# Optimization experiments

Hardware: AMD Instinct MI355X
Metric: run time of the kernel (lower is better)

The kernel has to match this reference:

```python
import jax, jax.numpy as jnp
import numpy as np

B, C, H, W = 32, 3, 224, 224
P = 16                 # patch size
D = 768                # embed_size
NH = 12                # num heads
HD = D // NH           # head size
L = 12                 # depth
MLP = 4 * D
NC = 1000              # num classes
GH, GW = H // P, W // P
T = GH * GW            # tokens = 196
PATCH_DIM = P * P * C
EPS = 1e-5


def posemb_sincos_2d(h, w, dim, temperature=10000.0):
    yy, xx = jnp.meshgrid(jnp.arange(h, dtype=jnp.float32),
                          jnp.arange(w, dtype=jnp.float32), indexing='ij')
    omega = jnp.arange(dim // 4, dtype=jnp.float32) / (dim // 4 - 1)
    omega = 1.0 / (temperature ** omega)
    yv = yy.reshape(-1)[:, None] * omega[None, :]
    xv = xx.reshape(-1)[:, None] * omega[None, :]
    return jnp.concatenate([jnp.sin(xv), jnp.cos(xv), jnp.sin(yv), jnp.cos(yv)], axis=1)


def layernorm(x, g, b):
    mu = jnp.mean(x, axis=-1, keepdims=True)
    var = jnp.mean((x - mu) ** 2, axis=-1, keepdims=True)
    return (x - mu) * jax.lax.rsqrt(var + EPS) * g + b


def setup_inputs() -> dict:
    key = jax.random.key(0)
    ks = jax.random.split(key, 16)
    s = 0.02
    inp = {
        'x': jax.random.normal(ks[0], (B, C, H, W), jnp.float32),
        'embed_W': jax.random.normal(ks[1], (PATCH_DIM, D), jnp.float32) * s,
        'embed_b': jnp.zeros((D,), jnp.float32),
        'Wq': jax.random.normal(ks[2], (L, NH, D, HD), jnp.float32) * s,
        'Wk': jax.random.normal(ks[3], (L, NH, D, HD), jnp.float32) * s,
        'Wv': jax.random.normal(ks[4], (L, NH, D, HD), jnp.float32) * s,
        'Wo': jax.random.normal(ks[5], (L, D, D), jnp.float32) * s,
        'bo': jnp.zeros((L, D), jnp.float32),
        'ln1_g': jnp.ones((L, D), jnp.float32),
        'ln1_b': jnp.zeros((L, D), jnp.float32),
        'ln2_g': jnp.ones((L, D), jnp.float32),
        'ln2_b': jnp.zeros((L, D), jnp.float32),
        'W1': jax.random.normal(ks[6], (L, D, MLP), jnp.float32) * s,
        'b1': jnp.zeros((L, MLP), jnp.float32),
        'W2': jax.random.normal(ks[7], (L, MLP, D), jnp.float32) * s,
        'b2': jnp.zeros((L, D), jnp.float32),
        'head_W': jax.random.normal(ks[8], (D, NC), jnp.float32) * s,
    }
    return inp


def reference(x, embed_W, embed_b, Wq, Wk, Wv, Wo, bo,
              ln1_g, ln1_b, ln2_g, ln2_b, W1, b1, W2, b2, head_W):
    # patchify: b c (h p1) (w p2) -> b (h w) (p1 p2 c)
    p = x.reshape(B, C, GH, P, GW, P)
    p = p.transpose(0, 2, 4, 3, 5, 1).reshape(B, T, PATCH_DIM)
    h = p @ embed_W + embed_b + posemb_sincos_2d(GH, GW, D)[None]  # [B,T,D]

    scale = HD ** -0.5
    for l in range(L):
        xn = layernorm(h, ln1_g[l], ln1_b[l])
        q = jnp.einsum('btd,hde->bhte', xn, Wq[l])
        k = jnp.einsum('btd,hde->bhte', xn, Wk[l])
        v = jnp.einsum('btd,hde->bhte', xn, Wv[l])
        scores = jax.nn.softmax(jnp.einsum('bhte,bhse->bhts', q, k) * scale, axis=-1)
        att = jnp.einsum('bhts,bhse->bhte', scores, v)
        att = att.transpose(0, 2, 1, 3).reshape(B, T, D)  # concat heads
        h = h + att @ Wo[l] + bo[l]
        xn = layernorm(h, ln2_g[l], ln2_b[l])
        h = h + jax.nn.gelu(xn @ W1[l] + b1[l], approximate=False) @ W2[l] + b2[l]

    return h.mean(axis=1) @ head_W  # [B, NC]
```

## Files before the change

kernel.cpp:

```cpp
#include <hip/hip_runtime.h>
#include <cstdint>


typedef __bf16 bf16_t;
typedef __bf16 bf16x8 __attribute__((ext_vector_type(8)));
typedef __bf16 bf16x4 __attribute__((ext_vector_type(4)));
typedef float  f32x4  __attribute__((ext_vector_type(4)));

#define NLAYER 12
#define BMPAD 56
#define PSTRIDE 4816896l

__device__ __forceinline__ void g2lds16(const void* g, void* l) {
  __builtin_amdgcn_global_load_lds(
      (const __attribute__((address_space(1))) void*)g,
      (__attribute__((address_space(3))) void*)l, 16, 0, 0);
}

__global__ __launch_bounds__(256) void tcvt(
    const float* __restrict__ in, bf16_t* __restrict__ out,
    int R, int C, long inStride, long outOuter, long outInner, int innerN)
{
  int bi = blockIdx.z;
  in  += (long)bi * inStride;
  out += (long)(bi / innerN) * outOuter + (long)(bi % innerN) * outInner;
  __shared__ float t[32][33];
  int c0 = blockIdx.x * 32, r0 = blockIdx.y * 32;
  int tx = threadIdx.x, ty = threadIdx.y;
  #pragma unroll
  for (int i = ty; i < 32; i += 8) {
    int r = r0 + i, c = c0 + tx;
    if (r < R && c < C) t[i][tx] = in[(long)r * C + c];
  }
  __syncthreads();
  #pragma unroll
  for (int i = ty; i < 32; i += 8) {
    int c = c0 + i, r = r0 + tx;
    if (r < R && c < C) out[(long)c * R + r] = (bf16_t)t[tx][i];
  }
}

__global__ __launch_bounds__(256) void patchify(
    const float* __restrict__ x, bf16_t* __restrict__ patches)
{
  int idx = blockIdx.x * 256 + threadIdx.x;
  int bt = idx / 768, pd = idx % 768;
  int b = bt / 196, t = bt % 196;
  int gh = t / 14, gw = t % 14;
  int p1 = pd / 48, rem = pd % 48;
  int p2 = rem / 3, c = rem % 3;
  float v = x[(((long)(b * 3 + c) * 224) + gh * 16 + p1) * 224 + gw * 16 + p2];
  patches[idx] = (bf16_t)v;
}

__global__ __launch_bounds__(256) void hinit(
    const float* __restrict__ eb, float* __restrict__ h)
{
  int idx = blockIdx.x * 256 + threadIdx.x;
  int t = idx / 768, d = idx % 768;
  int gh = t / 14, gw = t % 14;
  int quadrant = d / 192, i = d % 192;
  float omega = powf(10000.0f, -(float)i / 191.0f);
  float arg = (quadrant < 2 ? (float)gw : (float)gh) * omega;
  float pv = ((quadrant & 1) == 0) ? sinf(arg) : cosf(arg);
  float v = pv + eb[d];
  #pragma unroll
  for (int b = 0; b < 32; ++b) h[(long)b * 150528 + idx] = v;
}

__global__ __launch_bounds__(256) void ln_fuse(
    float* __restrict__ h, const bf16_t* __restrict__ pbuf, int nparts,
    const float* __restrict__ bias, const float* __restrict__ g,
    const float* __restrict__ bb, bf16_t* __restrict__ xn)
{
  int row = blockIdx.x * 4 + (threadIdx.x >> 6);
  int lane = threadIdx.x & 63;
  float* hr = h + (long)row * 768;
  const bf16_t* pr = pbuf + (long)row * 768;
  float4 v[3];
  float s = 0.f, s2 = 0.f;
  #pragma unroll
  for (int i = 0; i < 3; ++i) {
    int c4 = lane + 64 * i;
    float4 hv = ((const float4*)hr)[c4];
    float4 acc = {0.f, 0.f, 0.f, 0.f};
    for (int pp = 0; pp < nparts; ++pp) {
      bf16x4 q = *(const bf16x4*)(pr + (long)pp * PSTRIDE + c4 * 4);
      acc.x += (float)q[0]; acc.y += (float)q[1];
      acc.z += (float)q[2]; acc.w += (float)q[3];
    }
    if (bias) {
      float4 bv = ((const float4*)bias)[c4];
      acc.x += bv.x; acc.y += bv.y; acc.z += bv.z; acc.w += bv.w;
    }
    hv.x += acc.x; hv.y += acc.y; hv.z += acc.z; hv.w += acc.w;
    ((float4*)hr)[c4] = hv;
    v[i] = hv;
    s  += hv.x + hv.y + hv.z + hv.w;
    s2 += hv.x * hv.x + hv.y * hv.y + hv.z * hv.z + hv.w * hv.w;
  }
  #pragma unroll
  for (int d = 1; d < 64; d <<= 1) {
    s  += __shfl_xor(s, d, 64);
    s2 += __shfl_xor(s2, d, 64);
  }
  float mu = s * (1.0f / 768.0f);
  float var = s2 * (1.0f / 768.0f) - mu * mu;
  float rs = rsqrtf(var + 1e-5f);
  uint2* outv = (uint2*)(xn + (long)row * 768);
  const float4* gv = (const float4*)g;
  const float4* bv2 = (const float4*)bb;
  #pragma unroll
  for (int i = 0; i < 3; ++i) {
    int c4 = lane + 64 * i;
    float4 gg = gv[c4], b4 = bv2[c4];
    union { bf16_t q[4]; uint2 u; } pk;
    pk.q[0] = (bf16_t)((v[i].x - mu) * rs * gg.x + b4.x);
    pk.q[1] = (bf16_t)((v[i].y - mu) * rs * gg.y + b4.y);
    pk.q[2] = (bf16_t)((v[i].z - mu) * rs * gg.z + b4.z);
    pk.q[3] = (bf16_t)((v[i].w - mu) * rs * gg.w + b4.w);
    outv[c4] = pk.u;
  }
}

__device__ __forceinline__ float gelu_fast(float x) {
  float y = 0.7978845608f * (x + 0.044715f * x * x * x);
  float e = __expf(2.0f * y);
  float t = 1.0f - 2.0f / (e + 1.0f);
  return 0.5f * x * (1.0f + t);
}

template <int EPI, int KTOT, int KS>
__global__ __launch_bounds__(256, 4) void gemm_bt(
    const bf16_t* __restrict__ A, const bf16_t* __restrict__ Bt,
    int ldc, int Mstore, int Nstore,
    const float* __restrict__ bias,
    float* __restrict__ fout, bf16_t* __restrict__ bout)
{
  int lin = blockIdx.x;
  int bm = lin % BMPAD;
  if (bm * 128 >= Mstore) return;
  int rest = lin / BMPAD;
  int ks = rest % KS;
  int bn = rest / KS;
  constexpr int Ksl = KTOT / KS;
  int k0 = ks * Ksl;

  __shared__ __align__(16) bf16_t As[128 * 32];
  __shared__ __align__(16) bf16_t Bs[128 * 32];
  int tid = threadIdx.x;
  int wave = tid >> 6, lane = tid & 63, quad = lane >> 4, l16 = lane & 15;
  int wm = wave >> 1, wn = wave & 1;
  const bf16_t* Ab = A + (long)bm * 128 * KTOT;
  const bf16_t* Bb = Bt + (long)bn * 128 * KTOT;

  f32x4 zero = {0.f, 0.f, 0.f, 0.f};
  f32x4 acc[4][4];
  #pragma unroll
  for (int i = 0; i < 4; ++i)
    #pragma unroll
    for (int j = 0; j < 4; ++j) acc[i][j] = zero;

  int f0 = tid * 16;
  int row0 = f0 >> 6;
  int ke0 = (f0 & 63) >> 1;

  for (int kt = k0; kt < k0 + Ksl; kt += 32) {
    __syncthreads();
    g2lds16(Ab + (long)row0 * KTOT + kt + ke0,        (char*)As + f0);
    g2lds16(Ab + (long)(row0 + 64) * KTOT + kt + ke0, (char*)As + f0 + 4096);
    g2lds16(Bb + (long)row0 * KTOT + kt + ke0,        (char*)Bs + f0);
    g2lds16(Bb + (long)(row0 + 64) * KTOT + kt + ke0, (char*)Bs + f0 + 4096);
    __syncthreads();

    bf16x8 af[4], bfr[4];
    #pragma unroll
    for (int i = 0; i < 4; ++i)
      af[i] = *(const bf16x8*)(As + (wm * 64 + i * 16 + l16) * 32 + quad * 8);
    #pragma unroll
    for (int j = 0; j < 4; ++j)
      bfr[j] = *(const bf16x8*)(Bs + (wn * 64 + j * 16 + l16) * 32 + quad * 8);
    #pragma unroll
    for (int i = 0; i < 4; ++i)
      #pragma unroll
      for (int j = 0; j < 4; ++j)
        acc[i][j] = __builtin_amdgcn_mfma_f32_16x16x32_bf16(af[i], bfr[j], acc[i][j], 0, 0, 0);
  }

  int m0 = bm * 128 + wm * 64, n0 = bn * 128 + wn * 64;
  #pragma unroll
  for (int i = 0; i < 4; ++i)
    #pragma unroll
    for (int j = 0; j < 4; ++j)
      #pragma unroll
      for (int r = 0; r < 4; ++r) {
        int row = m0 + i * 16 + quad * 4 + r;
        int col = n0 + j * 16 + l16;
        if (row >= Mstore || col >= Nstore) continue;
        float v = acc[i][j][r];
        if (EPI == 0) {
          bout[(long)row * ldc + col] = (bf16_t)v;
        } else if (EPI == 3) {
          bout[(long)row * ldc + col] = (bf16_t)gelu_fast(v + bias[col]);
        } else if (EPI == 4) {
          fout[(long)row * ldc + col] = v;
        } else {
          bout[(long)ks * PSTRIDE + (long)row * ldc + col] = (bf16_t)v;
        }
      }
}

__global__ __launch_bounds__(256) void vtrans(
    const bf16_t* __restrict__ qkv, bf16_t* __restrict__ Vt)
{
  int bh = blockIdx.z, b = bh / 12, h = bh % 12;
  __shared__ bf16_t t[32][33];
  int e0 = blockIdx.x * 32, s0 = blockIdx.y * 32;
  int tx = threadIdx.x, ty = threadIdx.y;
  #pragma unroll
  for (int i = ty; i < 32; i += 8) {
    int s = s0 + i;
    bf16_t v = (bf16_t)0.0f;
    if (s < 196) v = qkv[(long)(b * 196 + s) * 2304 + 1536 + h * 64 + e0 + tx];
    t[i][tx] = v;
  }
  __syncthreads();
  #pragma unroll
  for (int i = ty; i < 32; i += 8) {
    int e = e0 + i, s = s0 + tx;
    if (s < 224) Vt[(long)bh * 64 * 224 + (long)e * 224 + s] = t[tx][i];
  }
}

__global__ __launch_bounds__(64) void attn_fused(
    const bf16_t* __restrict__ qkv, const bf16_t* __restrict__ Vt,
    bf16_t* __restrict__ att)
{
  __shared__ __align__(16) bf16_t Pl[16 * 232];
  int mt = blockIdx.x, bh = blockIdx.y;
  int b = bh / 12, h = bh % 12;
  int lane = threadIdx.x, quad = lane >> 4, l16 = lane & 15;

  #pragma unroll
  for (int i = 0; i < 4; ++i) {
    int idx = lane + 64 * i;
    Pl[(idx >> 4) * 232 + 208 + (idx & 15)] = (bf16_t)0.0f;
  }

  f32x4 zero = {0.f, 0.f, 0.f, 0.f};
  f32x4 acc[13];
  #pragma unroll
  for (int nt = 0; nt < 13; ++nt) acc[nt] = zero;

  long qoff = (long)(b * 196 + mt * 16 + l16) * 2304 + h * 64;
  #pragma unroll
  for (int kk = 0; kk < 2; ++kk) {
    bf16x8 a = *(const bf16x8*)(qkv + qoff + kk * 32 + quad * 8);
    #pragma unroll
    for (int nt = 0; nt < 13; ++nt) {
      long koff = (long)(b * 196 + nt * 16 + l16) * 2304 + 768 + h * 64 + kk * 32 + quad * 8;
      bf16x8 bb = *(const bf16x8*)(qkv + koff);
      acc[nt] = __builtin_amdgcn_mfma_f32_16x16x32_bf16(a, bb, acc[nt], 0, 0, 0);
    }
  }

  float p[13][4];
  #pragma unroll
  for (int nt = 0; nt < 13; ++nt)
    #pragma unroll
    for (int r = 0; r < 4; ++r) {
      float v = acc[nt][r] * 0.125f;
      if (nt == 12 && l16 >= 4) v = -1e30f;
      p[nt][r] = v;
    }

  #pragma unroll
  for (int r = 0; r < 4; ++r) {
    float mx = -1e30f;
    #pragma unroll
    for (int nt = 0; nt < 13; ++nt) mx = fmaxf(mx, p[nt][r]);
    #pragma unroll
    for (int d = 1; d < 16; d <<= 1) mx = fmaxf(mx, __shfl_xor(mx, d, 64));
    float sm = 0.f;
    #pragma unroll
    for (int nt = 0; nt < 13; ++nt) {
      float e = __expf(p[nt][r] - mx);
      p[nt][r] = e;
      sm += e;
    }
    #pragma unroll
    for (int d = 1; d < 16; d <<= 1) sm += __shfl_xor(sm, d, 64);
    float inv = 1.0f / sm;
    #pragma unroll
    for (int nt = 0; nt < 13; ++nt) p[nt][r] *= inv;
  }

  #pragma unroll
  for (int nt = 0; nt < 13; ++nt)
    #pragma unroll
    for (int r = 0; r < 4; ++r)
      Pl[(quad * 4 + r) * 232 + nt * 16 + l16] = (bf16_t)p[nt][r];
  __syncthreads();

  f32x4 pv[4];
  #pragma unroll
  for (int nt = 0; nt < 4; ++nt) pv[nt] = zero;
  const bf16_t* Vb = Vt + (long)bh * 64 * 224;
  #pragma unroll
  for (int ks = 0; ks < 7; ++ks) {
    bf16x8 a = *(const bf16x8*)(Pl + l16 * 232 + ks * 32 + quad * 8);
    #pragma unroll
    for (int nt = 0; nt < 4; ++nt) {
      bf16x8 bb = *(const bf16x8*)(Vb + (long)(nt * 16 + l16) * 224 + ks * 32 + quad * 8);
      pv[nt] = __builtin_amdgcn_mfma_f32_16x16x32_bf16(a, bb, pv[nt], 0, 0, 0);
    }
  }

  #pragma unroll
  for (int nt = 0; nt < 4; ++nt)
    #pragma unroll
    for (int r = 0; r < 4; ++r) {
      int t = mt * 16 + quad * 4 + r;
      if (t < 196)
        att[(long)(b * 196 + t) * 768 + h * 64 + nt * 16 + l16] = (bf16_t)pv[nt][r];
    }
}

__global__ __launch_bounds__(256) void meanpool_fuse(
    const float* __restrict__ h, const bf16_t* __restrict__ pbuf,
    const float* __restrict__ bias, bf16_t* __restrict__ hm)
{
  int d = blockIdx.y * 256 + threadIdx.x;
  int b = blockIdx.x;
  float s = 0.f;
  for (int t = 0; t < 196; ++t) {
    long idx = (long)(b * 196 + t) * 768 + d;
    float v = h[idx];
    #pragma unroll
    for (int pp = 0; pp < 4; ++pp) v += (float)pbuf[idx + pp * PSTRIDE];
    s += v;
  }
  hm[b * 768 + d] = (bf16_t)(s * (1.0f / 196.0f) + bias[d]);
}

extern "C" void kernel_launch(void* const* d_in, const int* in_sizes, int n_in,
                              void* d_out, int out_size, void* d_ws, size_t ws_size,
                              hipStream_t stream)
{
  const float* x       = (const float*)d_in[0];
  const float* embed_W = (const float*)d_in[1];
  const float* embed_b = (const float*)d_in[2];
  const float* Wq      = (const float*)d_in[3];
  const float* Wk      = (const float*)d_in[4];
  const float* Wv      = (const float*)d_in[5];
  const float* Wo      = (const float*)d_in[6];
  const float* bo      = (const float*)d_in[7];
  const float* ln1_g   = (const float*)d_in[8];
  const float* ln1_b   = (const float*)d_in[9];
  const float* ln2_g   = (const float*)d_in[10];
  const float* ln2_b   = (const float*)d_in[11];
  const float* W1      = (const float*)d_in[12];
  const float* b1      = (const float*)d_in[13];
  const float* W2      = (const float*)d_in[14];
  const float* b2      = (const float*)d_in[15];
  const float* head_W  = (const float*)d_in[16];

  char* p = (char*)d_ws;
  auto carve = [&](size_t bytes) {
    char* r = p;
    p += (bytes + 255) & ~(size_t)255;
    return r;
  };
  bf16_t* embed_Wt = (bf16_t*)carve(589824ull * 2);
  bf16_t* qkvT     = (bf16_t*)carve(21233664ull * 2);
  bf16_t* WoT      = (bf16_t*)carve(7077888ull * 2);
  bf16_t* W1T      = (bf16_t*)carve(28311552ull * 2);
  bf16_t* W2T      = (bf16_t*)carve(28311552ull * 2);
  bf16_t* headWt   = (bf16_t*)carve(786432ull * 2);
  bf16_t* patches  = (bf16_t*)carve(4816896ull * 2);
  float*  h        = (float*)carve(4816896ull * 4);
  bf16_t* xn       = (bf16_t*)carve(4816896ull * 2);
  bf16_t* qkv      = (bf16_t*)carve(14487552ull * 2);
  bf16_t* Vt       = (bf16_t*)carve(5505024ull * 2);
  bf16_t* hmlp     = (bf16_t*)carve(19267584ull * 2);
  bf16_t* att      = (bf16_t*)carve(4816896ull * 2);
  bf16_t* pbuf     = (bf16_t*)carve(4ull * PSTRIDE * 2);
  bf16_t* hm       = (bf16_t*)carve(98304ull * 2);
  (void)ws_size; (void)n_in; (void)in_sizes; (void)out_size;

  dim3 tb32(32, 8);

  tcvt<<<dim3(24, 24, 1),   tb32, 0, stream>>>(embed_W, embed_Wt, 768, 768, 0, 0, 0, 1);
  tcvt<<<dim3(24, 24, 12),  tb32, 0, stream>>>(Wo, WoT, 768, 768, 589824, 589824, 0, 1);
  tcvt<<<dim3(2, 24, 144),  tb32, 0, stream>>>(Wq, qkvT,           768, 64, 49152, 1769472, 49152, 12);
  tcvt<<<dim3(2, 24, 144),  tb32, 0, stream>>>(Wk, qkvT + 589824,  768, 64, 49152, 1769472, 49152, 12);
  tcvt<<<dim3(2, 24, 144),  tb32, 0, stream>>>(Wv, qkvT + 1179648, 768, 64, 49152, 1769472, 49152, 12);
  tcvt<<<dim3(96, 24, 12),  tb32, 0, stream>>>(W1, W1T, 768, 3072, 2359296, 2359296, 0, 1);
  tcvt<<<dim3(24, 96, 12),  tb32, 0, stream>>>(W2, W2T, 3072, 768, 2359296, 2359296, 0, 1);
  tcvt<<<dim3(32, 24, 1),   tb32, 0, stream>>>(head_W, headWt, 768, 1000, 0, 0, 0, 1);

  patchify<<<18816, 256, 0, stream>>>(x, patches);
  hinit<<<588, 256, 0, stream>>>(embed_b, h);

  gemm_bt<5, 768, 2><<<BMPAD * 6 * 2, 256, 0, stream>>>(
      patches, embed_Wt, 768, 6272, 768, nullptr, nullptr, pbuf);

  for (int l = 0; l < NLAYER; ++l) {
    ln_fuse<<<1568, 256, 0, stream>>>(
        h, pbuf, l == 0 ? 2 : 4, l == 0 ? nullptr : b2 + (l - 1) * 768,
        ln1_g + l * 768, ln1_b + l * 768, xn);
    gemm_bt<0, 768, 1><<<BMPAD * 18, 256, 0, stream>>>(
        xn, qkvT + (long)l * 1769472, 2304, 6272, 2304,
        nullptr, nullptr, qkv);
    vtrans<<<dim3(2, 7, 384), tb32, 0, stream>>>(qkv, Vt);
    attn_fused<<<dim3(13, 384), 64, 0, stream>>>(qkv, Vt, att);
    gemm_bt<5, 768, 2><<<BMPAD * 6 * 2, 256, 0, stream>>>(
        att, WoT + (long)l * 589824, 768, 6272, 768,
        nullptr, nullptr, pbuf);
    ln_fuse<<<1568, 256, 0, stream>>>(
        h, pbuf, 2, bo + l * 768, ln2_g + l * 768, ln2_b + l * 768, xn);
    gemm_bt<3, 768, 1><<<BMPAD * 24, 256, 0, stream>>>(
        xn, W1T + (long)l * 2359296, 3072, 6272, 3072,
        b1 + l * 3072, nullptr, hmlp);
    gemm_bt<5, 3072, 4><<<BMPAD * 6 * 4, 256, 0, stream>>>(
        hmlp, W2T + (long)l * 2359296, 768, 6272, 768,
        nullptr, nullptr, pbuf);
  }

  meanpool_fuse<<<dim3(32, 3), 256, 0, stream>>>(h, pbuf, b2 + 11 * 768, hm);
  gemm_bt<4, 768, 1><<<BMPAD * 8, 256, 0, stream>>>(
      hm, headWt, 1000, 32, 1000, nullptr, (float*)d_out, nullptr);
}
```

Measured before the change: 3.556 ms.

## Double GEMM K-tile to 64 and XOR-swizzle LDS layout

```diff
diff --git a/kernel.cpp b/kernel.cpp
--- a/kernel.cpp
+++ b/kernel.cpp
@@ -146,8 +146,8 @@
   constexpr int Ksl = KTOT / KS;
   int k0 = ks * Ksl;
 
-  __shared__ __align__(16) bf16_t As[128 * 32];
-  __shared__ __align__(16) bf16_t Bs[128 * 32];
+  __shared__ __align__(16) bf16_t As[128 * 64];
+  __shared__ __align__(16) bf16_t Bs[128 * 64];
   int tid = threadIdx.x;
   int wave = tid >> 6, lane = tid & 63, quad = lane >> 4, l16 = lane & 15;
   int wm = wave >> 1, wn = wave & 1;
@@ -161,30 +161,47 @@
     #pragma unroll
     for (int j = 0; j < 4; ++j) acc[i][j] = zero;
 
-  int f0 = tid * 16;
-  int row0 = f0 >> 6;
-  int ke0 = (f0 & 63) >> 1;
-
-  for (int kt = k0; kt < k0 + Ksl; kt += 32) {
+  int srow = tid >> 3;
+  int sgcol = ((tid & 7) ^ (srow & 7)) * 8;
+  int ldst = tid * 16;
+
+  int aoff[2][4], boff[2][4];
+  #pragma unroll
+  for (int kh = 0; kh < 2; ++kh)
+    #pragma unroll
+    for (int i = 0; i < 4; ++i) {
+      int ra = wm * 64 + i * 16 + l16;
+      int rb = wn * 64 + i * 16 + l16;
+      int pa = ((kh * 4 + quad) ^ (ra & 7)) * 8;
+      int pb = ((kh * 4 + quad) ^ (rb & 7)) * 8;
+      aoff[kh][i] = ra * 64 + pa;
+      boff[kh][i] = rb * 64 + pb;
+    }
+
+  for (int kt = k0; kt < k0 + Ksl; kt += 64) {
     __syncthreads();
-    g2lds16(Ab + (long)row0 * KTOT + kt + ke0,        (char*)As + f0);
-    g2lds16(Ab + (long)(row0 + 64) * KTOT + kt + ke0, (char*)As + f0 + 4096);
-    g2lds16(Bb + (long)row0 * KTOT + kt + ke0,        (char*)Bs + f0);
-    g2lds16(Bb + (long)(row0 + 64) * KTOT + kt + ke0, (char*)Bs + f0 + 4096);
+    #pragma unroll
+    for (int c = 0; c < 4; ++c) {
+      g2lds16(Ab + (long)(c * 32 + srow) * KTOT + kt + sgcol,
+              (char*)As + c * 4096 + ldst);
+      g2lds16(Bb + (long)(c * 32 + srow) * KTOT + kt + sgcol,
+              (char*)Bs + c * 4096 + ldst);
+    }
     __syncthreads();
 
-    bf16x8 af[4], bfr[4];
-    #pragma unroll
-    for (int i = 0; i < 4; ++i)
-      af[i] = *(const bf16x8*)(As + (wm * 64 + i * 16 + l16) * 32 + quad * 8);
-    #pragma unroll
-    for (int j = 0; j < 4; ++j)
-      bfr[j] = *(const bf16x8*)(Bs + (wn * 64 + j * 16 + l16) * 32 + quad * 8);
-    #pragma unroll
-    for (int i = 0; i < 4; ++i)
+    #pragma unroll
+    for (int kh = 0; kh < 2; ++kh) {
+      bf16x8 af[4], bfr[4];
       #pragma unroll
-      for (int j = 0; j < 4; ++j)
-        acc[i][j] = __builtin_amdgcn_mfma_f32_16x16x32_bf16(af[i], bfr[j], acc[i][j], 0, 0, 0);
+      for (int i = 0; i < 4; ++i) af[i] = *(const bf16x8*)(As + aoff[kh][i]);
+      #pragma unroll
+      for (int j = 0; j < 4; ++j) bfr[j] = *(const bf16x8*)(Bs + boff[kh][j]);
+      #pragma unroll
+      for (int i = 0; i < 4; ++i)
+        #pragma unroll
+        for (int j = 0; j < 4; ++j)
+          acc[i][j] = __builtin_amdgcn_mfma_f32_16x16x32_bf16(af[i], bfr[j], acc[i][j], 0, 0, 0);
+    }
   }
 
   int m0 = bm * 128 + wm * 64, n0 = bn * 128 + wn * 64;
```

After: 3.292 ms. 7.4% less time.

## Double-buffer GEMM LDS with XOR swizzle and fuse V transpose into QKV epilogue

Applied to the files above, without the earlier changes.

```diff
diff --git a/kernel.cpp b/kernel.cpp
--- a/kernel.cpp
+++ b/kernel.cpp
@@ -66,6 +66,13 @@
   float v = pv + eb[d];
   #pragma unroll
   for (int b = 0; b < 32; ++b) h[(long)b * 150528 + idx] = v;
+}
+
+__global__ __launch_bounds__(256) void vpad(bf16_t* __restrict__ Vt)
+{
+  int i = blockIdx.x * 256 + threadIdx.x;
+  int s = 196 + (i % 28), rest = i / 28;
+  Vt[(long)rest * 224 + s] = (bf16_t)0.0f;
 }
 
 __global__ __launch_bounds__(256) void ln_fuse(
@@ -135,7 +142,8 @@
     const bf16_t* __restrict__ A, const bf16_t* __restrict__ Bt,
     int ldc, int Mstore, int Nstore,
     const float* __restrict__ bias,
-    float* __restrict__ fout, bf16_t* __restrict__ bout)
+    float* __restrict__ fout, bf16_t* __restrict__ bout,
+    bf16_t* __restrict__ vout)
 {
   int lin = blockIdx.x;
   int bm = lin % BMPAD;
@@ -144,15 +152,16 @@
   int ks = rest % KS;
   int bn = rest / KS;
   constexpr int Ksl = KTOT / KS;
+  constexpr int NIT = Ksl / 32;
   int k0 = ks * Ksl;
 
-  __shared__ __align__(16) bf16_t As[128 * 32];
-  __shared__ __align__(16) bf16_t Bs[128 * 32];
+  __shared__ __align__(16) bf16_t As[2][128 * 32];
+  __shared__ __align__(16) bf16_t Bs[2][128 * 32];
   int tid = threadIdx.x;
   int wave = tid >> 6, lane = tid & 63, quad = lane >> 4, l16 = lane & 15;
   int wm = wave >> 1, wn = wave & 1;
-  const bf16_t* Ab = A + (long)bm * 128 * KTOT;
-  const bf16_t* Bb = Bt + (long)bn * 128 * KTOT;
+  const bf16_t* Ab = A + (long)bm * 128 * KTOT + k0;
+  const bf16_t* Bb = Bt + (long)bn * 128 * KTOT + k0;
 
   f32x4 zero = {0.f, 0.f, 0.f, 0.f};
   f32x4 acc[4][4];
@@ -161,25 +170,40 @@
     #pragma unroll
     for (int j = 0; j < 4; ++j) acc[i][j] = zero;
 
-  int f0 = tid * 16;
-  int row0 = f0 >> 6;
-  int ke0 = (f0 & 63) >> 1;
-
-  for (int kt = k0; kt < k0 + Ksl; kt += 32) {
+  int srow = tid >> 2;
+  int sgcol = ((tid & 3) ^ ((srow >> 1) & 3)) * 8;
+  int ldst = tid * 16;
+  long ag0 = (long)srow * KTOT + sgcol;
+  long ag1 = (long)(64 + srow) * KTOT + sgcol;
+
+  int physf = (quad ^ ((l16 >> 1) & 3)) * 8;
+  int aoff[4], boff[4];
+  #pragma unroll
+  for (int i = 0; i < 4; ++i) {
+    aoff[i] = (wm * 64 + i * 16 + l16) * 32 + physf;
+    boff[i] = (wn * 64 + i * 16 + l16) * 32 + physf;
+  }
+
+  g2lds16(Ab + ag0, (char*)As[0] + ldst);
+  g2lds16(Ab + ag1, (char*)As[0] + 4096 + ldst);
+  g2lds16(Bb + ag0, (char*)Bs[0] + ldst);
+  g2lds16(Bb + ag1, (char*)Bs[0] + 4096 + ldst);
+
+  for (int it = 0; it < NIT; ++it) {
+    int cur = it & 1;
     __syncthreads();
-    g2lds16(Ab + (long)row0 * KTOT + kt + ke0,        (char*)As + f0);
-    g2lds16(Ab + (long)(row0 + 64) * KTOT + kt + ke0, (char*)As + f0 + 4096);
-    g2lds16(Bb + (long)row0 * KTOT + kt + ke0,        (char*)Bs + f0);
-    g2lds16(Bb + (long)(row0 + 64) * KTOT + kt + ke0, (char*)Bs + f0 + 4096);
-    __syncthreads();
-
+    if (it + 1 < NIT) {
+      int kt = (it + 1) * 32;
+      g2lds16(Ab + ag0 + kt, (char*)As[cur ^ 1] + ldst);
+      g2lds16(Ab + ag1 + kt, (char*)As[cur ^ 1] + 4096 + ldst);
+      g2lds16(Bb + ag0 + kt, (char*)Bs[cur ^ 1] + ldst);
+      g2lds16(Bb + ag1 + kt, (char*)Bs[cur ^ 1] + 4096 + ldst);
+    }
     bf16x8 af[4], bfr[4];
     #pragma unroll
-    for (int i = 0; i < 4; ++i)
-      af[i] = *(const bf16x8*)(As + (wm * 64 + i * 16 + l16) * 32 + quad * 8);
-    #pragma unroll
-    for (int j = 0; j < 4; ++j)
-      bfr[j] = *(const bf16x8*)(Bs + (wn * 64 + j * 16 + l16) * 32 + quad * 8);
+    for (int i = 0; i < 4; ++i) af[i] = *(const bf16x8*)(As[cur] + aoff[i]);
+    #pragma unroll
+    for (int j = 0; j < 4; ++j) bfr[j] = *(const bf16x8*)(Bs[cur] + boff[j]);
     #pragma unroll
     for (int i = 0; i < 4; ++i)
       #pragma unroll
@@ -204,32 +228,18 @@
           bout[(long)row * ldc + col] = (bf16_t)gelu_fast(v + bias[col]);
         } else if (EPI == 4) {
           fout[(long)row * ldc + col] = v;
+        } else if (EPI == 5) {
+          bout[(long)ks * PSTRIDE + (long)row * ldc + col] = (bf16_t)v;
         } else {
-          bout[(long)ks * PSTRIDE + (long)row * ldc + col] = (bf16_t)v;
+          if (col < 1536) {
+            bout[(long)row * ldc + col] = (bf16_t)v;
+          } else {
+            int hh = (col - 1536) >> 6, e = (col - 1536) & 63;
+            int bb2 = row / 196, s = row - bb2 * 196;
+            vout[((long)(bb2 * 12 + hh) * 64 + e) * 224 + s] = (bf16_t)v;
+          }
         }
       }
-}
-
-__global__ __launch_bounds__(256) void vtrans(
-    const bf16_t* __restrict__ qkv, bf16_t* __restrict__ Vt)
-{
-  int bh = blockIdx.z, b = bh / 12, h = bh % 12;
-  __shared__ bf16_t t[32][33];
-  int e0 = blockIdx.x * 32, s0 = blockIdx.y * 32;
-  int tx = threadIdx.x, ty = threadIdx.y;
-  #pragma unroll
-  for (int i = ty; i < 32; i += 8) {
-    int s = s0 + i;
-    bf16_t v = (bf16_t)0.0f;
-    if (s < 196) v = qkv[(long)(b * 196 + s) * 2304 + 1536 + h * 64 + e0 + tx];
-    t[i][tx] = v;
-  }
-  __syncthreads();
-  #pragma unroll
-  for (int i = ty; i < 32; i += 8) {
-    int e = e0 + i, s = s0 + tx;
-    if (s < 224) Vt[(long)bh * 64 * 224 + (long)e * 224 + s] = t[tx][i];
-  }
 }
 
 __global__ __launch_bounds__(64) void attn_fused(
@@ -401,33 +411,33 @@
 
   patchify<<<18816, 256, 0, stream>>>(x, patches);
   hinit<<<588, 256, 0, stream>>>(embed_b, h);
+  vpad<<<2688, 256, 0, stream>>>(Vt);
 
   gemm_bt<5, 768, 2><<<BMPAD * 6 * 2, 256, 0, stream>>>(
-      patches, embed_Wt, 768, 6272, 768, nullptr, nullptr, pbuf);
+      patches, embed_Wt, 768, 6272, 768, nullptr, nullptr, pbuf, nullptr);
 
   for (int l = 0; l < NLAYER; ++l) {
     ln_fuse<<<1568, 256, 0, stream>>>(
         h, pbuf, l == 0 ? 2 : 4, l == 0 ? nullptr : b2 + (l - 1) * 768,
         ln1_g + l * 768, ln1_b + l * 768, xn);
-    gemm_bt<0, 768, 1><<<BMPAD * 18, 256, 0, stream>>>(
+    gemm_bt<6, 768, 1><<<BMPAD * 18, 256, 0, stream>>>(
         xn, qkvT + (long)l * 1769472, 2304, 6272, 2304,
-        nullptr, nullptr, qkv);
-    vtrans<<<dim3(2, 7, 384), tb32, 0, stream>>>(qkv, Vt);
+        nullptr, nullptr, qkv, Vt);
     attn_fused<<<dim3(13, 384), 64, 0, stream>>>(qkv, Vt, att);
     gemm_bt<5, 768, 2><<<BMPAD * 6 * 2, 256, 0, stream>>>(
         att, WoT + (long)l * 589824, 768, 6272, 768,
-        nullptr, nullptr, pbuf);
+        nullptr, nullptr, pbuf, nullptr);
     ln_fuse<<<1568, 256, 0, stream>>>(
         h, pbuf, 2, bo + l * 768, ln2_g + l * 768, ln2_b + l * 768, xn);
     gemm_bt<3, 768, 1><<<BMPAD * 24, 256, 0, stream>>>(
         xn, W1T + (long)l * 2359296, 3072, 6272, 3072,
-        b1 + l * 3072, nullptr, hmlp);
+        b1 + l * 3072, nullptr, hmlp, nullptr);
     gemm_bt<5, 3072, 4><<<BMPAD * 6 * 4, 256, 0, stream>>>(
         hmlp, W2T + (long)l * 2359296, 768, 6272, 768,
-        nullptr, nullptr, pbuf);
+        nullptr, nullptr, pbuf, nullptr);
   }
 
   meanpool_fuse<<<dim3(32, 3), 256, 0, stream>>>(h, pbuf, b2 + 11 * 768, hm);
   gemm_bt<4, 768, 1><<<BMPAD * 8, 256, 0, stream>>>(
-      hm, headWt, 1000, 32, 1000, nullptr, (float*)d_out, nullptr);
-}
+      hm, headWt, 1000, 32, 1000, nullptr, (float*)d_out, nullptr, nullptr);
+}
```

After: 3.765 ms. 5.9% more time.
